# Optimization experiments

Measured on AMD Instinct MI355X. Metric: run time of the kernel, lower is better.

Reference implementation:

```python
import jax, jax.numpy as jnp
import numpy as np

N_NODES = 30460
D = 64
B = 128
K = 6924          # candidates per group (ReDial movie set)
S = B * K
M_PER = 50
M = B * M_PER
A_HID = 20


def setup_inputs() -> dict:
    key = jax.random.key(0)
    ks = jax.random.split(key, 16)
    inp = {}
    inp["graph_embed"] = jax.random.normal(ks[0], (N_NODES, D), jnp.float32) * 0.1
    inp["utterance_embed"] = jax.random.normal(ks[1], (B, D), jnp.float32) * 0.1
    inp["abstract_embed"] = jnp.zeros((1, D), jnp.float32)
    inp["Wa"] = jax.random.normal(ks[2], (D, A_HID), jnp.float32) * 0.1
    inp["Va"] = jax.random.normal(ks[3], (A_HID, 1), jnp.float32) * 0.1
    inp["W1w"] = jax.random.normal(ks[4], (3, 192), jnp.float32) * 0.05
    inp["W1b"] = jnp.zeros((3,), jnp.float32)
    inp["W2w"] = jax.random.normal(ks[5], (3, 192), jnp.float32) * 0.05
    inp["W2b"] = jnp.zeros((3,), jnp.float32)
    inp["mention_index"] = jax.random.randint(ks[6], (M,), 0, N_NODES)
    inp["mention_batch_index"] = jnp.repeat(jnp.arange(B), M_PER)
    for l, (k_sel, k_last, k_int) in enumerate([(ks[7], ks[8], ks[9]), (ks[10], ks[11], ks[12])]):
        inp[f"sel_index{l}"] = jax.random.randint(k_sel, (S,), 0, N_NODES + 1)
        inp[f"sel_batch_index{l}"] = jnp.repeat(jnp.arange(B), K)
        inp[f"sel_group_index{l}"] = jnp.repeat(jnp.arange(B), K)
        inp[f"grp_batch_index{l}"] = jnp.arange(B)
        inp[f"last_index{l}"] = jax.random.randint(k_last, (B,), 0, N_NODES + 1)
        inp[f"intent_index{l}"] = jax.random.randint(k_int, (B,), 0, 3)
    return inp


def _user_portrait(graph_embed, Wa, Va, mention_index, mention_batch_index):
    # Self_Attention with scatter-softmax over mention groups
    me = graph_embed[mention_index]                       # [M, D]
    beta = (jnp.tanh(me @ Wa) @ Va)[:, 0]                  # [M]
    exp_b = jnp.exp(beta)
    denom = jax.ops.segment_sum(exp_b, mention_batch_index, num_segments=B)
    alpha = exp_b / denom[mention_batch_index]             # [M]
    return jax.ops.segment_sum(alpha[:, None] * me, mention_batch_index, num_segments=B)  # [B, D]


def _layer(utter, portrait, ge, Ww, Wb, sel, sel_bat, sel_grp, grp_bat, last, intent):
    feats = ge[sel]                                        # [S, D]
    ctx = jnp.concatenate([utter, portrait], axis=-1)[grp_bat]   # [G, 2D] (tile_context == gather)
    start = ge[last]                                       # [G, D]
    grp_ctx = jnp.concatenate([ctx, start], axis=-1)       # [G, 3D]
    w_all = jax.nn.sigmoid(grp_ctx @ Ww.T + Wb)            # [G, 3] chat/question/recommend
    w = jnp.take_along_axis(w_all, intent[:, None], axis=1)  # [G, 1]
    tw = w[sel_grp]                                        # [S, 1]
    q = utter[sel_bat] * tw + portrait[sel_bat] * (1.0 - tw)  # [S, D]
    return jnp.sum(q * feats, axis=-1)                     # [S]


def reference(graph_embed, utterance_embed, abstract_embed, Wa, Va, W1w, W1b, W2w, W2b,
              mention_index, mention_batch_index,
              sel_index0, sel_batch_index0, sel_group_index0, grp_batch_index0, last_index0, intent_index0,
              sel_index1, sel_batch_index1, sel_group_index1, grp_batch_index1, last_index1, intent_index1):
    portrait = _user_portrait(graph_embed, Wa, Va, mention_index, mention_batch_index)
    ge = jnp.concatenate([graph_embed, abstract_embed], axis=0)  # [N+1, D]
    s0 = _layer(utterance_embed, portrait, ge, W1w, W1b,
                sel_index0, sel_batch_index0, sel_group_index0, grp_batch_index0, last_index0, intent_index0)
    s1 = _layer(utterance_embed, portrait, ge, W2w, W2b,
                sel_index1, sel_batch_index1, sel_group_index1, grp_batch_index1, last_index1, intent_index1)
    return jnp.stack([s0, s1])                              # [2, S]
```

## Files before the change

kernel.cpp:

```cpp
#include <hip/hip_runtime.h>
#include <cmath>

#define N_NODES 30460
#define D 64
#define B 128
#define K_SEL 6924
#define S_TOT (B * K_SEL)
#define NPAD 30464
#define NB_CHUNKS 238

#define WS_PORT 0
#define WS_TW   (B * D)
#define WS_TAB  (B * D + 2 * B)

typedef _Float16 half_t;
typedef _Float16 half8 __attribute__((ext_vector_type(8)));
typedef float f32x4 __attribute__((ext_vector_type(4)));
typedef float f32x2 __attribute__((ext_vector_type(2)));

#define STRG 136
#define STRX 72

__global__ __launch_bounds__(256) void k_port(
    const float* __restrict__ graph, const float* __restrict__ abs_e,
    const float* __restrict__ utter,
    const float* __restrict__ Wa, const float* __restrict__ Va,
    const float* __restrict__ W1w, const float* __restrict__ W1b,
    const float* __restrict__ W2w, const float* __restrict__ W2b,
    const int* __restrict__ midx,
    const int* __restrict__ la0, const int* __restrict__ it0,
    const int* __restrict__ la1, const int* __restrict__ it1,
    float* __restrict__ ws) {
    __shared__ float sWa[D * 24];
    __shared__ float sVa[20];
    __shared__ float sExp[4][64];
    __shared__ int   sIdx[4][64];
    int t = threadIdx.x, wave = t >> 6, lane = t & 63;
    for (int i = t; i < D * 20; i += 256) {
        int d = i / 20, j = i - d * 20;
        sWa[d * 24 + j] = Wa[i];
    }
    if (t < 20) sVa[t] = Va[t];
    __syncthreads();

    int b = blockIdx.x * 4 + wave;
    float e = 0.f; int mi = 0;
    if (lane < 50) {
        mi = midx[b * 50 + lane];
        const float* me = graph + (size_t)mi * D;
        float h[20];
#pragma unroll
        for (int j = 0; j < 20; j++) h[j] = 0.f;
#pragma unroll 2
        for (int d4 = 0; d4 < 16; ++d4) {
            float4 v = *(const float4*)(me + d4 * 4);
            const float* wb = &sWa[(d4 * 4) * 24];
#pragma unroll
            for (int e2 = 0; e2 < 4; ++e2) {
                float vv = (e2 == 0) ? v.x : (e2 == 1) ? v.y : (e2 == 2) ? v.z : v.w;
                const float* wr = wb + e2 * 24;
#pragma unroll
                for (int j4 = 0; j4 < 5; ++j4) {
                    float4 w = *(const float4*)(wr + j4 * 4);
                    h[j4 * 4 + 0] += vv * w.x;
                    h[j4 * 4 + 1] += vv * w.y;
                    h[j4 * 4 + 2] += vv * w.z;
                    h[j4 * 4 + 3] += vv * w.w;
                }
            }
        }
        float beta = 0.f;
#pragma unroll
        for (int j = 0; j < 20; j++) beta += tanhf(h[j]) * sVa[j];
        e = expf(beta);
    }
    sExp[wave][lane] = e;
    sIdx[wave][lane] = mi;
    __syncthreads();

    float x = e;
    x += __shfl_xor(x, 32, 64); x += __shfl_xor(x, 16, 64);
    x += __shfl_xor(x, 8, 64);  x += __shfl_xor(x, 4, 64);
    x += __shfl_xor(x, 2, 64);  x += __shfl_xor(x, 1, 64);

    float acc = 0.f;
#pragma unroll 5
    for (int m = 0; m < 50; m++)
        acc += sExp[wave][m] * graph[(size_t)sIdx[wave][m] * D + lane];
    float p = acc / x;
    ws[WS_PORT + b * D + lane] = p;
    float u = utter[(size_t)b * D + lane];

#pragma unroll
    for (int l = 0; l < 2; ++l) {
        const int* lap = l ? la1 : la0;
        const int* itp = l ? it1 : it0;
        const float* Ww = l ? W2w : W1w;
        const float* Wb = l ? W2b : W1b;
        int li = lap[b], it = itp[b];
        const float* wr = Ww + it * 3 * D;
        float sv = (li < N_NODES) ? graph[(size_t)li * D + lane] : abs_e[lane];
        float a = wr[lane] * u + wr[D + lane] * p + wr[2 * D + lane] * sv;
        a += __shfl_xor(a, 32, 64); a += __shfl_xor(a, 16, 64);
        a += __shfl_xor(a, 8, 64);  a += __shfl_xor(a, 4, 64);
        a += __shfl_xor(a, 2, 64);  a += __shfl_xor(a, 1, 64);
        if (lane == 0) ws[WS_TW + l * B + b] = 1.f / (1.f + expf(-(a + Wb[it])));
    }
}

__global__ __launch_bounds__(256) void k_table(
    const float* __restrict__ graph, const float* __restrict__ abs_e,
    const float* __restrict__ utter, float* __restrict__ ws) {
    __shared__ half_t Gs[128 * STRG];
    __shared__ half_t Xs[256 * STRX];
    const int nb = blockIdx.x, t = threadIdx.x;
    const float* port = ws + WS_PORT;

#pragma unroll
    for (int pz = 0; pz < 2; ++pz) {
        int row = pz * 64 + (t >> 2), q = t & 3;
        int n = nb * 128 + row;
        const float* src = ((n < N_NODES) ? (graph + (size_t)n * D) : abs_e) + q * 16;
        half_t* dh = &Gs[row * STRG + q * 16];
        half_t* dl = dh + 64;
        float4 f0 = *(const float4*)(src);
        float4 f1 = *(const float4*)(src + 4);
        float4 f2 = *(const float4*)(src + 8);
        float4 f3 = *(const float4*)(src + 12);
        half8 hh, ll;
        hh[0]=(half_t)f0.x; hh[1]=(half_t)f0.y; hh[2]=(half_t)f0.z; hh[3]=(half_t)f0.w;
        hh[4]=(half_t)f1.x; hh[5]=(half_t)f1.y; hh[6]=(half_t)f1.z; hh[7]=(half_t)f1.w;
        ll[0]=(half_t)((f0.x-(float)hh[0])*4096.f); ll[1]=(half_t)((f0.y-(float)hh[1])*4096.f);
        ll[2]=(half_t)((f0.z-(float)hh[2])*4096.f); ll[3]=(half_t)((f0.w-(float)hh[3])*4096.f);
        ll[4]=(half_t)((f1.x-(float)hh[4])*4096.f); ll[5]=(half_t)((f1.y-(float)hh[5])*4096.f);
        ll[6]=(half_t)((f1.z-(float)hh[6])*4096.f); ll[7]=(half_t)((f1.w-(float)hh[7])*4096.f);
        *(half8*)(dh) = hh; *(half8*)(dl) = ll;
        hh[0]=(half_t)f2.x; hh[1]=(half_t)f2.y; hh[2]=(half_t)f2.z; hh[3]=(half_t)f2.w;
        hh[4]=(half_t)f3.x; hh[5]=(half_t)f3.y; hh[6]=(half_t)f3.z; hh[7]=(half_t)f3.w;
        ll[0]=(half_t)((f2.x-(float)hh[0])*4096.f); ll[1]=(half_t)((f2.y-(float)hh[1])*4096.f);
        ll[2]=(half_t)((f2.z-(float)hh[2])*4096.f); ll[3]=(half_t)((f2.w-(float)hh[3])*4096.f);
        ll[4]=(half_t)((f3.x-(float)hh[4])*4096.f); ll[5]=(half_t)((f3.y-(float)hh[5])*4096.f);
        ll[6]=(half_t)((f3.z-(float)hh[6])*4096.f); ll[7]=(half_t)((f3.w-(float)hh[7])*4096.f);
        *(half8*)(dh + 8) = hh; *(half8*)(dl + 8) = ll;
    }
#pragma unroll
    for (int pz = 0; pz < 2; ++pz) {
        int row = pz * 128 + (t >> 1), c = t & 1;
        const float* src = ((row < 128) ? (utter + (size_t)row * D)
                                        : (port + (size_t)(row - 128) * D)) + c * 32;
        half_t* dx = &Xs[row * STRX + c * 32];
#pragma unroll
        for (int g = 0; g < 4; ++g) {
            float4 f0 = *(const float4*)(src + g * 8);
            float4 f1 = *(const float4*)(src + g * 8 + 4);
            half8 hh;
            hh[0]=(half_t)f0.x; hh[1]=(half_t)f0.y; hh[2]=(half_t)f0.z; hh[3]=(half_t)f0.w;
            hh[4]=(half_t)f1.x; hh[5]=(half_t)f1.y; hh[6]=(half_t)f1.z; hh[7]=(half_t)f1.w;
            *(half8*)(dx + g * 8) = hh;
        }
    }
    __syncthreads();

    const int wv = t >> 6, m16 = t & 15, kq = (t & 63) >> 4;
    float2* tab = (float2*)(ws + WS_TAB);
    const f32x4 zero = {0.f, 0.f, 0.f, 0.f};

#pragma unroll
    for (int pp = 0; pp < 2; ++pp) {
        int pi = wv * 2 + pp;
        int ru = pi * 16 + m16, rp = 128 + pi * 16 + m16;
        half8 au0 = *(half8*)&Xs[ru * STRX + kq * 8];
        half8 au1 = *(half8*)&Xs[ru * STRX + 32 + kq * 8];
        half8 ap0 = *(half8*)&Xs[rp * STRX + kq * 8];
        half8 ap1 = *(half8*)&Xs[rp * STRX + 32 + kq * 8];
#pragma unroll
        for (int nt = 0; nt < 8; ++nt) {
            int n16 = nt * 16 + m16;
            const half_t* gr = &Gs[n16 * STRG + kq * 8];
            half8 bh0 = *(half8*)(gr);
            half8 bh1 = *(half8*)(gr + 32);
            half8 bl0 = *(half8*)(gr + 64);
            half8 bl1 = *(half8*)(gr + 96);
            f32x4 aU = zero, aUl = zero, aP = zero, aPl = zero;
            aU  = __builtin_amdgcn_mfma_f32_16x16x32_f16(au0, bh0, aU, 0, 0, 0);
            aU  = __builtin_amdgcn_mfma_f32_16x16x32_f16(au1, bh1, aU, 0, 0, 0);
            aUl = __builtin_amdgcn_mfma_f32_16x16x32_f16(au0, bl0, aUl, 0, 0, 0);
            aUl = __builtin_amdgcn_mfma_f32_16x16x32_f16(au1, bl1, aUl, 0, 0, 0);
            aP  = __builtin_amdgcn_mfma_f32_16x16x32_f16(ap0, bh0, aP, 0, 0, 0);
            aP  = __builtin_amdgcn_mfma_f32_16x16x32_f16(ap1, bh1, aP, 0, 0, 0);
            aPl = __builtin_amdgcn_mfma_f32_16x16x32_f16(ap0, bl0, aPl, 0, 0, 0);
            aPl = __builtin_amdgcn_mfma_f32_16x16x32_f16(ap1, bl1, aPl, 0, 0, 0);
            int n = nb * 128 + n16;
#pragma unroll
            for (int r = 0; r < 4; ++r) {
                int b = pi * 16 + kq * 4 + r;
                float u  = aU[r] + aUl[r] * 2.44140625e-4f;
                float pv = aP[r] + aPl[r] * 2.44140625e-4f;
                tab[(size_t)b * NPAD + n] = make_float2(u, pv);
            }
        }
    }
}

__global__ __launch_bounds__(256) void k_out(
    const int* __restrict__ si0, const int* __restrict__ si1,
    const float* __restrict__ ws, float* __restrict__ out) {
    const int l = blockIdx.y;
    const int* __restrict__ si = l ? si1 : si0;
    const float2* __restrict__ tab = (const float2*)(ws + WS_TAB);
    int s0 = (blockIdx.x * 256 + threadIdx.x) * 2;
    int2 id = *(const int2*)(si + s0);
    unsigned bat = (unsigned)s0 / (unsigned)K_SEL;
    float tw = ws[WS_TW + l * B + bat];
    float2 v0 = tab[(size_t)bat * NPAD + id.x];
    float2 v1 = tab[(size_t)bat * NPAD + id.y];
    f32x2 r;
    r.x = v0.y + tw * (v0.x - v0.y);
    r.y = v1.y + tw * (v1.x - v1.y);
    __builtin_nontemporal_store(r, (f32x2*)&out[(size_t)l * S_TOT + s0]);
}

extern "C" void kernel_launch(void* const* d_in, const int* in_sizes, int n_in,
                              void* d_out, int out_size, void* d_ws, size_t ws_size,
                              hipStream_t stream) {
    const float* graph = (const float*)d_in[0];
    const float* utter = (const float*)d_in[1];
    const float* abs_e = (const float*)d_in[2];
    const float* Wa    = (const float*)d_in[3];
    const float* Va    = (const float*)d_in[4];
    const float* W1w   = (const float*)d_in[5];
    const float* W1b   = (const float*)d_in[6];
    const float* W2w   = (const float*)d_in[7];
    const float* W2b   = (const float*)d_in[8];
    const int* midx = (const int*)d_in[9];
    const int* si0 = (const int*)d_in[11];
    const int* la0 = (const int*)d_in[15];
    const int* it0 = (const int*)d_in[16];
    const int* si1 = (const int*)d_in[17];
    const int* la1 = (const int*)d_in[21];
    const int* it1 = (const int*)d_in[22];

    float* ws = (float*)d_ws;

    k_port<<<32, 256, 0, stream>>>(graph, abs_e, utter, Wa, Va,
                                   W1w, W1b, W2w, W2b, midx,
                                   la0, it0, la1, it1, ws);

    k_table<<<NB_CHUNKS, 256, 0, stream>>>(graph, abs_e, utter, ws);

    dim3 grid(S_TOT / 512, 2);
    k_out<<<grid, 256, 0, stream>>>(si0, si1, ws, (float*)d_out);
}
```

Measured before the change: 156.8 us.

## Store score table in fp16, drop split-precision MFMA, remap output blocks per XCD

Removes the hi/lo fp16 split of graph embeddings, so the table kernel runs half the MFMAs and half the LDS traffic. The table is written as packed half2 instead of float2, which halves the table write and the gathered reads in the output kernel. The output grid becomes 1D with an XCD-aware remapping so that consecutive work items, which share a batch's table rows, land on the same XCD's L2. The portrait gather loop is also unrolled further. The risk is lower precision, since scores now carry fp16 input rounding and fp16 storage error.

```diff
diff --git a/kernel.cpp b/kernel.cpp
--- a/kernel.cpp
+++ b/kernel.cpp
@@ -8,6 +8,7 @@
 #define S_TOT (B * K_SEL)
 #define NPAD 30464
 #define NB_CHUNKS 238
+#define NWG_OUT 3462
 
 #define WS_PORT 0
 #define WS_TW   (B * D)
@@ -15,10 +16,11 @@
 
 typedef _Float16 half_t;
 typedef _Float16 half8 __attribute__((ext_vector_type(8)));
+typedef _Float16 half2_t __attribute__((ext_vector_type(2)));
 typedef float f32x4 __attribute__((ext_vector_type(4)));
 typedef float f32x2 __attribute__((ext_vector_type(2)));
 
-#define STRG 136
+#define STRG 72
 #define STRX 72
 
 __global__ __launch_bounds__(256) void k_port(
@@ -84,7 +86,7 @@
     x += __shfl_xor(x, 2, 64);  x += __shfl_xor(x, 1, 64);
 
     float acc = 0.f;
-#pragma unroll 5
+#pragma unroll 10
     for (int m = 0; m < 50; m++)
         acc += sExp[wave][m] * graph[(size_t)sIdx[wave][m] * D + lane];
     float p = acc / x;
@@ -122,26 +124,17 @@
         int n = nb * 128 + row;
         const float* src = ((n < N_NODES) ? (graph + (size_t)n * D) : abs_e) + q * 16;
         half_t* dh = &Gs[row * STRG + q * 16];
-        half_t* dl = dh + 64;
         float4 f0 = *(const float4*)(src);
         float4 f1 = *(const float4*)(src + 4);
         float4 f2 = *(const float4*)(src + 8);
         float4 f3 = *(const float4*)(src + 12);
-        half8 hh, ll;
+        half8 hh;
         hh[0]=(half_t)f0.x; hh[1]=(half_t)f0.y; hh[2]=(half_t)f0.z; hh[3]=(half_t)f0.w;
         hh[4]=(half_t)f1.x; hh[5]=(half_t)f1.y; hh[6]=(half_t)f1.z; hh[7]=(half_t)f1.w;
-        ll[0]=(half_t)((f0.x-(float)hh[0])*4096.f); ll[1]=(half_t)((f0.y-(float)hh[1])*4096.f);
-        ll[2]=(half_t)((f0.z-(float)hh[2])*4096.f); ll[3]=(half_t)((f0.w-(float)hh[3])*4096.f);
-        ll[4]=(half_t)((f1.x-(float)hh[4])*4096.f); ll[5]=(half_t)((f1.y-(float)hh[5])*4096.f);
-        ll[6]=(half_t)((f1.z-(float)hh[6])*4096.f); ll[7]=(half_t)((f1.w-(float)hh[7])*4096.f);
-        *(half8*)(dh) = hh; *(half8*)(dl) = ll;
+        *(half8*)(dh) = hh;
         hh[0]=(half_t)f2.x; hh[1]=(half_t)f2.y; hh[2]=(half_t)f2.z; hh[3]=(half_t)f2.w;
         hh[4]=(half_t)f3.x; hh[5]=(half_t)f3.y; hh[6]=(half_t)f3.z; hh[7]=(half_t)f3.w;
-        ll[0]=(half_t)((f2.x-(float)hh[0])*4096.f); ll[1]=(half_t)((f2.y-(float)hh[1])*4096.f);
-        ll[2]=(half_t)((f2.z-(float)hh[2])*4096.f); ll[3]=(half_t)((f2.w-(float)hh[3])*4096.f);
-        ll[4]=(half_t)((f3.x-(float)hh[4])*4096.f); ll[5]=(half_t)((f3.y-(float)hh[5])*4096.f);
-        ll[6]=(half_t)((f3.z-(float)hh[6])*4096.f); ll[7]=(half_t)((f3.w-(float)hh[7])*4096.f);
-        *(half8*)(dh + 8) = hh; *(half8*)(dl + 8) = ll;
+        *(half8*)(dh + 8) = hh;
     }
 #pragma unroll
     for (int pz = 0; pz < 2; ++pz) {
@@ -162,7 +155,7 @@
     __syncthreads();
 
     const int wv = t >> 6, m16 = t & 15, kq = (t & 63) >> 4;
-    float2* tab = (float2*)(ws + WS_TAB);
+    half2_t* tabh = (half2_t*)(ws + WS_TAB);
     const f32x4 zero = {0.f, 0.f, 0.f, 0.f};
 
 #pragma unroll
@@ -179,24 +172,19 @@
             const half_t* gr = &Gs[n16 * STRG + kq * 8];
             half8 bh0 = *(half8*)(gr);
             half8 bh1 = *(half8*)(gr + 32);
-            half8 bl0 = *(half8*)(gr + 64);
-            half8 bl1 = *(half8*)(gr + 96);
-            f32x4 aU = zero, aUl = zero, aP = zero, aPl = zero;
-            aU  = __builtin_amdgcn_mfma_f32_16x16x32_f16(au0, bh0, aU, 0, 0, 0);
-            aU  = __builtin_amdgcn_mfma_f32_16x16x32_f16(au1, bh1, aU, 0, 0, 0);
-            aUl = __builtin_amdgcn_mfma_f32_16x16x32_f16(au0, bl0, aUl, 0, 0, 0);
-            aUl = __builtin_amdgcn_mfma_f32_16x16x32_f16(au1, bl1, aUl, 0, 0, 0);
-            aP  = __builtin_amdgcn_mfma_f32_16x16x32_f16(ap0, bh0, aP, 0, 0, 0);
-            aP  = __builtin_amdgcn_mfma_f32_16x16x32_f16(ap1, bh1, aP, 0, 0, 0);
-            aPl = __builtin_amdgcn_mfma_f32_16x16x32_f16(ap0, bl0, aPl, 0, 0, 0);
-            aPl = __builtin_amdgcn_mfma_f32_16x16x32_f16(ap1, bl1, aPl, 0, 0, 0);
+            f32x4 aU = zero, aP = zero;
+            aU = __builtin_amdgcn_mfma_f32_16x16x32_f16(au0, bh0, aU, 0, 0, 0);
+            aU = __builtin_amdgcn_mfma_f32_16x16x32_f16(au1, bh1, aU, 0, 0, 0);
+            aP = __builtin_amdgcn_mfma_f32_16x16x32_f16(ap0, bh0, aP, 0, 0, 0);
+            aP = __builtin_amdgcn_mfma_f32_16x16x32_f16(ap1, bh1, aP, 0, 0, 0);
             int n = nb * 128 + n16;
 #pragma unroll
             for (int r = 0; r < 4; ++r) {
                 int b = pi * 16 + kq * 4 + r;
-                float u  = aU[r] + aUl[r] * 2.44140625e-4f;
-                float pv = aP[r] + aPl[r] * 2.44140625e-4f;
-                tab[(size_t)b * NPAD + n] = make_float2(u, pv);
+                half2_t hv;
+                hv[0] = (half_t)aU[r];
+                hv[1] = (half_t)aP[r];
+                tabh[(size_t)b * NPAD + n] = hv;
             }
         }
     }
@@ -205,19 +193,27 @@
 __global__ __launch_bounds__(256) void k_out(
     const int* __restrict__ si0, const int* __restrict__ si1,
     const float* __restrict__ ws, float* __restrict__ out) {
-    const int l = blockIdx.y;
+    const int w = blockIdx.x;
+    const int q = NWG_OUT / 8, r = NWG_OUT % 8;
+    int xcd = w & 7, j = w >> 3;
+    int work = (xcd < r ? xcd * (q + 1) : r * (q + 1) + (xcd - r) * q) + j;
+    const int l = work & 1;
+    const int x = work >> 1;
+
     const int* __restrict__ si = l ? si1 : si0;
-    const float2* __restrict__ tab = (const float2*)(ws + WS_TAB);
-    int s0 = (blockIdx.x * 256 + threadIdx.x) * 2;
+    const half2_t* __restrict__ tabh = (const half2_t*)(ws + WS_TAB);
+    int s0 = (x * 256 + threadIdx.x) * 2;
     int2 id = *(const int2*)(si + s0);
     unsigned bat = (unsigned)s0 / (unsigned)K_SEL;
     float tw = ws[WS_TW + l * B + bat];
-    float2 v0 = tab[(size_t)bat * NPAD + id.x];
-    float2 v1 = tab[(size_t)bat * NPAD + id.y];
-    f32x2 r;
-    r.x = v0.y + tw * (v0.x - v0.y);
-    r.y = v1.y + tw * (v1.x - v1.y);
-    __builtin_nontemporal_store(r, (f32x2*)&out[(size_t)l * S_TOT + s0]);
+    half2_t v0 = tabh[(size_t)bat * NPAD + id.x];
+    half2_t v1 = tabh[(size_t)bat * NPAD + id.y];
+    f32x2 rr;
+    float u0 = (float)v0[0], p0 = (float)v0[1];
+    float u1 = (float)v1[0], p1 = (float)v1[1];
+    rr.x = p0 + tw * (u0 - p0);
+    rr.y = p1 + tw * (u1 - p1);
+    __builtin_nontemporal_store(rr, (f32x2*)&out[(size_t)l * S_TOT + s0]);
 }
 
 extern "C" void kernel_launch(void* const* d_in, const int* in_sizes, int n_in,
@@ -248,6 +244,5 @@
 
     k_table<<<NB_CHUNKS, 256, 0, stream>>>(graph, abs_e, utter, ws);
 
-    dim3 grid(S_TOT / 512, 2);
-    k_out<<<grid, 256, 0, stream>>>(si0, si1, ws, (float*)d_out);
-}
+    k_out<<<NWG_OUT, 256, 0, stream>>>(si0, si1, ws, (float*)d_out);
+}
```

New measurement: 137.0 us. 12.6% less time.
